# Optimization experiments

Hardware: AMD Instinct MI355X
Metric: run time of the kernel (lower is better)

## Reference

```python
import jax, jax.numpy as jnp
import numpy as np

B, S, H, NH = 2, 2048, 2048, 16
HD = H // NH
SCALE = 1.0 / np.sqrt(HD).astype(np.float32)


def setup_inputs() -> dict:
    key = jax.random.key(0)
    ks = jax.random.split(key, 11)
    std = 1.0 / np.sqrt(H)
    inp = {
        'query': jax.random.normal(ks[0], (B, S, H), dtype=jnp.float32),
        'key': jax.random.normal(ks[1], (B, S, H), dtype=jnp.float32),
        'value': jax.random.normal(ks[2], (B, S, H), dtype=jnp.float32),
        'Wq': jax.random.normal(ks[3], (H, H), dtype=jnp.float32) * std,
        'bq': jax.random.normal(ks[4], (H,), dtype=jnp.float32) * std,
        'Wk': jax.random.normal(ks[5], (H, H), dtype=jnp.float32) * std,
        'bk': jax.random.normal(ks[6], (H,), dtype=jnp.float32) * std,
        'Wv': jax.random.normal(ks[7], (H, H), dtype=jnp.float32) * std,
        'bv': jax.random.normal(ks[8], (H,), dtype=jnp.float32) * std,
        'Wo': jax.random.normal(ks[9], (H, H), dtype=jnp.float32) * std,
        'bo': jax.random.normal(ks[10], (H,), dtype=jnp.float32) * std,
    }
    return inp


def reference(query, key, value, Wq, bq, Wk, bk, Wv, bv, Wo, bo):
    # Linear projections (torch Linear: x @ W.T + b)
    q = query @ Wq.T + bq
    k = key @ Wk.T + bk
    v = value @ Wv.T + bv
    # [B, NH, S, HD]
    q = q.reshape(B, S, NH, HD).transpose(0, 2, 1, 3)
    k = k.reshape(B, S, NH, HD).transpose(0, 2, 1, 3)
    v = v.reshape(B, S, NH, HD).transpose(0, 2, 1, 3)
    scores = jnp.einsum('bhqd,bhkd->bhqk', q, k) * SCALE
    attn = jax.nn.softmax(scores, axis=-1)  # dropout p=0 (eval)
    ctx = jnp.einsum('bhqk,bhkd->bhqd', attn, v)
    ctx = ctx.transpose(0, 2, 1, 3).reshape(B, S, H)
    out = ctx @ Wo.T + bo
    return out
```

## Files before the change

kernel.cpp:

```cpp
#include <hip/hip_runtime.h>


typedef __bf16 bf16_t;
typedef __bf16 bf16x8 __attribute__((ext_vector_type(8)));
typedef float  f32x4  __attribute__((ext_vector_type(4)));

#define DEVI __device__ __forceinline__

DEVI void async_copy16(const void* gsrc, void* ldst) {
  __builtin_amdgcn_global_load_lds(
      (const __attribute__((address_space(1))) unsigned int*)gsrc,
      (__attribute__((address_space(3))) unsigned int*)ldst, 16, 0, 0);
}

constexpr int Bc = 2, Sc = 2048, Hc = 2048, NHc = 16, HDc = 128;
constexpr float SCALE_F = 0.088388347648318447f;
constexpr int PSTR = 72;

DEVI void cast_body(const float* __restrict__ in, bf16_t* __restrict__ out) {
  int i = (blockIdx.x * 256 + threadIdx.x) * 8;
  float4 f0 = *(const float4*)(in + i);
  float4 f1 = *(const float4*)(in + i + 4);
  union { bf16_t h[8]; uint4 u; } o;
  o.h[0] = (bf16_t)f0.x; o.h[1] = (bf16_t)f0.y;
  o.h[2] = (bf16_t)f0.z; o.h[3] = (bf16_t)f0.w;
  o.h[4] = (bf16_t)f1.x; o.h[5] = (bf16_t)f1.y;
  o.h[6] = (bf16_t)f1.z; o.h[7] = (bf16_t)f1.w;
  *(uint4*)(out + i) = o.u;
}

__global__ void cast3(const float* __restrict__ a, const float* __restrict__ b,
                      const float* __restrict__ c, bf16_t* __restrict__ oa,
                      bf16_t* __restrict__ ob, bf16_t* __restrict__ oc) {
  const float* src = blockIdx.y == 0 ? a : blockIdx.y == 1 ? b : c;
  bf16_t* dst = blockIdx.y == 0 ? oa : blockIdx.y == 1 ? ob : oc;
  cast_body(src, dst);
}

__global__ void cast4(const float* __restrict__ a, const float* __restrict__ b,
                      const float* __restrict__ c, const float* __restrict__ d,
                      bf16_t* __restrict__ oa, bf16_t* __restrict__ ob,
                      bf16_t* __restrict__ oc, bf16_t* __restrict__ od) {
  const float* src = blockIdx.y == 0 ? a : blockIdx.y == 1 ? b
                   : blockIdx.y == 2 ? c : d;
  bf16_t* dst = blockIdx.y == 0 ? oa : blockIdx.y == 1 ? ob
              : blockIdx.y == 2 ? oc : od;
  cast_body(src, dst);
}

template <int M, int N, int K, int OUT_MODE>
__global__ __launch_bounds__(512, 2) void gemm_bt(const bf16_t* __restrict__ A,
                                                  const bf16_t* __restrict__ Bw,
                                                  const float* __restrict__ bias,
                                                  void* __restrict__ Cout,
                                                  float scale) {
  constexpr int BM = 256, BN = 128, BK = 64;
  constexpr int NT = K / BK;
  constexpr int SLOT = (BM + BN) * BK;
  __shared__ __align__(16) bf16_t lds[3 * SLOT];

  const int tid = threadIdx.x;
  const int lane = tid & 63;
  const int wave = tid >> 6;
  const int bm = blockIdx.x & (M / BM - 1);
  const int bn = blockIdx.x / (M / BM);
  const int wm = wave >> 1, wn = wave & 1;
  const int quad = lane >> 4, l15 = lane & 15;

  const bf16_t* Abase = A + (size_t)bm * BM * K;
  const bf16_t* Bbase = Bw + (size_t)bn * BN * K;
  const bf16_t* asrc0; const bf16_t* asrc1; const bf16_t* asrc2; const bf16_t* asrc3;
  const bf16_t* bsrc0; const bf16_t* bsrc1;
  int aoff0, aoff1, aoff2, aoff3, boff0, boff1;
  {
    int i0 = wave * 4;
    int r0 = i0 * 8 + (lane >> 3);       aoff0 = i0 * 512;
    int r1 = (i0 + 1) * 8 + (lane >> 3); aoff1 = (i0 + 1) * 512;
    int r2 = (i0 + 2) * 8 + (lane >> 3); aoff2 = (i0 + 2) * 512;
    int r3 = (i0 + 3) * 8 + (lane >> 3); aoff3 = (i0 + 3) * 512;
    asrc0 = Abase + (size_t)r0 * K + (((lane & 7) ^ (r0 & 7)) * 8);
    asrc1 = Abase + (size_t)r1 * K + (((lane & 7) ^ (r1 & 7)) * 8);
    asrc2 = Abase + (size_t)r2 * K + (((lane & 7) ^ (r2 & 7)) * 8);
    asrc3 = Abase + (size_t)r3 * K + (((lane & 7) ^ (r3 & 7)) * 8);
    int j0 = wave * 2;
    int s0 = j0 * 8 + (lane >> 3);       boff0 = BM * BK + j0 * 512;
    int s1 = (j0 + 1) * 8 + (lane >> 3); boff1 = BM * BK + (j0 + 1) * 512;
    bsrc0 = Bbase + (size_t)s0 * K + (((lane & 7) ^ (s0 & 7)) * 8);
    bsrc1 = Bbase + (size_t)s1 * K + (((lane & 7) ^ (s1 & 7)) * 8);
  }

  f32x4 zero4 = {0.f, 0.f, 0.f, 0.f};
  f32x4 acc[4][4];
#pragma unroll
  for (int i = 0; i < 4; ++i)
#pragma unroll
    for (int j = 0; j < 4; ++j) acc[i][j] = zero4;

  int arow[4], brow[4];
#pragma unroll
  for (int t = 0; t < 4; ++t) {
    arow[t] = wm * 64 + t * 16 + l15;
    brow[t] = wn * 64 + t * 16 + l15;
  }

  auto stage_half0 = [&](int kt) {
    bf16_t* slot = lds + (kt % 3) * SLOT;
    int k0 = kt * BK;
    async_copy16(asrc0 + k0, slot + aoff0);
    async_copy16(asrc1 + k0, slot + aoff1);
    async_copy16(bsrc0 + k0, slot + boff0);
  };
  auto stage_half1 = [&](int kt) {
    bf16_t* slot = lds + (kt % 3) * SLOT;
    int k0 = kt * BK;
    async_copy16(asrc2 + k0, slot + aoff2);
    async_copy16(asrc3 + k0, slot + aoff3);
    async_copy16(bsrc1 + k0, slot + boff1);
  };

  stage_half0(0); stage_half1(0);
  stage_half0(1); stage_half1(1);

  for (int kt = 0; kt < NT; ++kt) {
    if (kt + 1 < NT) {
      asm volatile("s_waitcnt vmcnt(6)" ::: "memory");
    } else {
      asm volatile("s_waitcnt vmcnt(0)" ::: "memory");
    }
    __builtin_amdgcn_s_barrier();
    asm volatile("" ::: "memory");

    const bf16_t* As = lds + (kt % 3) * SLOT;
    const bf16_t* Bs = As + BM * BK;
    const bool do_stage = (kt + 2 < NT);

#pragma unroll
    for (int ks = 0; ks < 2; ++ks) {
      if (do_stage) {
        if (ks == 0) stage_half0(kt + 2);
        else         stage_half1(kt + 2);
      }
      bf16x8 af[4], bfv[4];
#pragma unroll
      for (int mt = 0; mt < 4; ++mt)
        af[mt] = *(const bf16x8*)(As + arow[mt] * 64 +
                                  (((ks * 4 + quad) ^ (arow[mt] & 7)) * 8));
#pragma unroll
      for (int nt = 0; nt < 4; ++nt)
        bfv[nt] = *(const bf16x8*)(Bs + brow[nt] * 64 +
                                   (((ks * 4 + quad) ^ (brow[nt] & 7)) * 8));
      __builtin_amdgcn_s_setprio(1);
#pragma unroll
      for (int mt = 0; mt < 4; ++mt)
#pragma unroll
        for (int nt = 0; nt < 4; ++nt)
          acc[mt][nt] = __builtin_amdgcn_mfma_f32_16x16x32_bf16(
              af[mt], bfv[nt], acc[mt][nt], 0, 0, 0);
      __builtin_amdgcn_s_setprio(0);
    }
  }

  float bv[4];
#pragma unroll
  for (int nt = 0; nt < 4; ++nt) bv[nt] = bias[bn * BN + brow[nt]];

#pragma unroll
  for (int mt = 0; mt < 4; ++mt) {
    const int rbase = bm * BM + wm * 64 + mt * 16 + quad * 4;
#pragma unroll
    for (int nt = 0; nt < 4; ++nt) {
      const int col = bn * BN + brow[nt];
      if constexpr (OUT_MODE == 0) {
        bf16_t* C = (bf16_t*)Cout;
#pragma unroll
        for (int r = 0; r < 4; ++r)
          C[(size_t)(rbase + r) * N + col] = (bf16_t)((acc[mt][nt][r] + bv[nt]) * scale);
      } else if constexpr (OUT_MODE == 2) {
        float* C = (float*)Cout;
#pragma unroll
        for (int r = 0; r < 4; ++r)
          C[(size_t)(rbase + r) * N + col] = acc[mt][nt][r] + bv[nt];
      } else {
        bf16_t* C = (bf16_t*)Cout;
        const int bb = rbase >> 11;
        const int s0 = rbase & (Sc - 1);
        const int h = col >> 7, d = col & (HDc - 1);
        union { bf16_t h4[4]; uint2 u; } o;
#pragma unroll
        for (int r = 0; r < 4; ++r) o.h4[r] = (bf16_t)(acc[mt][nt][r] + bv[nt]);
        *(uint2*)(C + (((size_t)(bb * NHc + h) * HDc + d) * Sc + s0)) = o.u;
      }
    }
  }
}

__global__ __launch_bounds__(256, 2) void flash_attn(const bf16_t* __restrict__ Q,
                                                     const bf16_t* __restrict__ Kg,
                                                     const bf16_t* __restrict__ Vt,
                                                     bf16_t* __restrict__ ctx) {
  __shared__ __align__(16) bf16_t smem[64 * 128 + 128 * 64 + 4 * 32 * PSTR];
  bf16_t* Ks = smem;
  bf16_t* Vs = smem + 8192;
  bf16_t* Ps = smem + 16384;

  const int tid = threadIdx.x, lane = tid & 63, wave = tid >> 6;
  const int quad = lane >> 4, l15 = lane & 15;
  const int bid = blockIdx.x;
  const int qt = bid & 15, h = (bid >> 4) & 15, b = bid >> 8;

  bf16_t* Pw = Ps + wave * (32 * PSTR);

  bf16x8 qf[2][4];
#pragma unroll
  for (int mt = 0; mt < 2; ++mt) {
    int grow = b * Sc + qt * 128 + wave * 32 + mt * 16 + l15;
    const bf16_t* qp = Q + (size_t)grow * Hc + h * HDc;
#pragma unroll
    for (int kc = 0; kc < 4; ++kc) qf[mt][kc] = *(const bf16x8*)(qp + kc * 32 + quad * 8);
  }

  f32x4 zero4 = {0.f, 0.f, 0.f, 0.f};
  f32x4 o[2][8];
#pragma unroll
  for (int mt = 0; mt < 2; ++mt)
#pragma unroll
    for (int dt = 0; dt < 8; ++dt) o[mt][dt] = zero4;
  float mrow[2][4], lrow[2][4];
#pragma unroll
  for (int mt = 0; mt < 2; ++mt)
#pragma unroll
    for (int r = 0; r < 4; ++r) { mrow[mt][r] = -1e30f; lrow[mt][r] = 0.f; }

  int kr_[4], kc_[4], vr_[4], vc_[4];
#pragma unroll
  for (int i = 0; i < 4; ++i) {
    int s = wave * 4 + i;
    kr_[i] = s * 4 + quad;        kc_[i] = l15 ^ (kr_[i] & 7);
    vr_[i] = s * 8 + (lane >> 3); vc_[i] = (lane & 7) ^ (vr_[i] & 7);
  }
  const bf16_t* Kbase = Kg + (size_t)b * Sc * Hc + h * HDc;
  const bf16_t* Vbase = Vt + (size_t)(b * NHc + h) * HDc * Sc;

  for (int kb = 0; kb < 32; ++kb) {
#pragma unroll
    for (int i = 0; i < 4; ++i) {
      int s = wave * 4 + i;
      async_copy16(Kbase + (size_t)(kb * 64 + kr_[i]) * Hc + kc_[i] * 8, Ks + s * 512);
      async_copy16(Vbase + (size_t)vr_[i] * Sc + kb * 64 + vc_[i] * 8, Vs + s * 512);
    }
    __syncthreads();

    f32x4 sf[2][4];
#pragma unroll
    for (int mt = 0; mt < 2; ++mt)
#pragma unroll
      for (int nt = 0; nt < 4; ++nt) sf[mt][nt] = zero4;
#pragma unroll
    for (int kc = 0; kc < 4; ++kc)
#pragma unroll
      for (int nt = 0; nt < 4; ++nt) {
        int kr = nt * 16 + l15;
        bf16x8 kf = *(const bf16x8*)(Ks + kr * 128 + (((kc * 4 + quad) ^ (kr & 7)) * 8));
        sf[0][nt] = __builtin_amdgcn_mfma_f32_16x16x32_bf16(qf[0][kc], kf, sf[0][nt], 0, 0, 0);
        sf[1][nt] = __builtin_amdgcn_mfma_f32_16x16x32_bf16(qf[1][kc], kf, sf[1][nt], 0, 0, 0);
      }

#pragma unroll
    for (int mt = 0; mt < 2; ++mt)
#pragma unroll
      for (int r = 0; r < 4; ++r) {
        float mx = sf[mt][0][r];
#pragma unroll
        for (int nt = 1; nt < 4; ++nt) mx = fmaxf(mx, sf[mt][nt][r]);
#pragma unroll
        for (int off = 1; off < 16; off <<= 1) mx = fmaxf(mx, __shfl_xor(mx, off));
        float mnew = fmaxf(mrow[mt][r], mx);
        float alpha = __expf(mrow[mt][r] - mnew);
        float rs = 0.f;
#pragma unroll
        for (int nt = 0; nt < 4; ++nt) {
          float p = __expf(sf[mt][nt][r] - mnew);
          sf[mt][nt][r] = p;
          rs += p;
        }
#pragma unroll
        for (int off = 1; off < 16; off <<= 1) rs += __shfl_xor(rs, off);
        lrow[mt][r] = lrow[mt][r] * alpha + rs;
        mrow[mt][r] = mnew;
#pragma unroll
        for (int dt = 0; dt < 8; ++dt) o[mt][dt][r] *= alpha;
      }

#pragma unroll
    for (int mt = 0; mt < 2; ++mt)
#pragma unroll
      for (int nt = 0; nt < 4; ++nt)
#pragma unroll
        for (int r = 0; r < 4; ++r)
          Pw[(mt * 16 + quad * 4 + r) * PSTR + nt * 16 + l15] = (bf16_t)sf[mt][nt][r];

    bf16x8 pf[2][2];
#pragma unroll
    for (int mt = 0; mt < 2; ++mt) {
      const bf16_t* pr = Pw + (mt * 16 + l15) * PSTR;
#pragma unroll
      for (int kc = 0; kc < 2; ++kc)
        pf[mt][kc] = *(const bf16x8*)(pr + kc * 32 + quad * 8);
    }

#pragma unroll
    for (int kc = 0; kc < 2; ++kc)
#pragma unroll
      for (int dt = 0; dt < 8; ++dt) {
        int vr = dt * 16 + l15;
        bf16x8 vf = *(const bf16x8*)(Vs + vr * 64 + (((kc * 4 + quad) ^ (vr & 7)) * 8));
        o[0][dt] = __builtin_amdgcn_mfma_f32_16x16x32_bf16(pf[0][kc], vf, o[0][dt], 0, 0, 0);
        o[1][dt] = __builtin_amdgcn_mfma_f32_16x16x32_bf16(pf[1][kc], vf, o[1][dt], 0, 0, 0);
      }
    __syncthreads();
  }

  __syncthreads();
  bf16_t* Ow = smem + wave * 4096;
#pragma unroll
  for (int mt = 0; mt < 2; ++mt) {
    float rinv[4];
#pragma unroll
    for (int r = 0; r < 4; ++r) rinv[r] = 1.f / lrow[mt][r];
#pragma unroll
    for (int dt = 0; dt < 8; ++dt)
#pragma unroll
      for (int r = 0; r < 4; ++r)
        Ow[(mt * 16 + quad * 4 + r) * 128 + dt * 16 + l15] = (bf16_t)(o[mt][dt][r] * rinv[r]);
  }
#pragma unroll
  for (int r = 0; r < 32; ++r) {
    unsigned v = *(const unsigned*)(Ow + r * 128 + lane * 2);
    int grow = b * Sc + qt * 128 + wave * 32 + r;
    *(unsigned*)(ctx + (size_t)grow * Hc + h * HDc + lane * 2) = v;
  }
}

extern "C" void kernel_launch(void* const* d_in, const int* in_sizes, int n_in,
                              void* d_out, int out_size, void* d_ws, size_t ws_size,
                              hipStream_t stream) {
  const float* query = (const float*)d_in[0];
  const float* key_i = (const float*)d_in[1];
  const float* value = (const float*)d_in[2];
  const float* Wq = (const float*)d_in[3];
  const float* bq = (const float*)d_in[4];
  const float* Wk = (const float*)d_in[5];
  const float* bk = (const float*)d_in[6];
  const float* Wv = (const float*)d_in[7];
  const float* bv = (const float*)d_in[8];
  const float* Wo = (const float*)d_in[9];
  const float* bo = (const float*)d_in[10];

  const size_t XE = (size_t)Bc * Sc * Hc;
  const size_t WE = (size_t)Hc * Hc;
  const size_t need = 6 * XE * 2 + 4 * WE * 2;
  if (ws_size < need) return;

  char* ws = (char*)d_ws;
  size_t off = 0;
  auto alloc = [&](size_t bytes) {
    char* p = ws + off;
    off += (bytes + 255) & ~(size_t)255;
    return p;
  };
  bf16_t* Xq = (bf16_t*)alloc(XE * 2);
  bf16_t* Xk = (bf16_t*)alloc(XE * 2);
  bf16_t* Xv = (bf16_t*)alloc(XE * 2);
  bf16_t* Wqb = (bf16_t*)alloc(WE * 2);
  bf16_t* Wkb = (bf16_t*)alloc(WE * 2);
  bf16_t* Wvb = (bf16_t*)alloc(WE * 2);
  bf16_t* Wob = (bf16_t*)alloc(WE * 2);
  bf16_t* qb = (bf16_t*)alloc(XE * 2);
  bf16_t* kb = (bf16_t*)alloc(XE * 2);
  bf16_t* vtb = (bf16_t*)alloc(XE * 2);
  bf16_t* ctxb = Xq;

  cast3<<<dim3((unsigned)(XE / 2048), 3), 256, 0, stream>>>(query, key_i, value, Xq, Xk, Xv);
  cast4<<<dim3((unsigned)(WE / 2048), 4), 256, 0, stream>>>(Wq, Wk, Wv, Wo, Wqb, Wkb, Wvb, Wob);

  gemm_bt<4096, 2048, 2048, 0><<<256, 512, 0, stream>>>(Xq, Wqb, bq, qb, SCALE_F);
  gemm_bt<4096, 2048, 2048, 0><<<256, 512, 0, stream>>>(Xk, Wkb, bk, kb, 1.0f);
  gemm_bt<4096, 2048, 2048, 1><<<256, 512, 0, stream>>>(Xv, Wvb, bv, vtb, 1.0f);

  flash_attn<<<512, 256, 0, stream>>>(qb, kb, vtb, ctxb);

  gemm_bt<4096, 2048, 2048, 2><<<256, 512, 0, stream>>>(ctxb, Wob, bo, (float*)d_out, 1.0f);
}
```

Before: 474.4 us.

## Merge QKV GEMMs into one launch and pipeline flash attention with lazy rescaling

The three Q/K/V projection GEMMs become a single launch with a 3-way grid, which fills the GPU with 768 blocks instead of three 256-block waves. Flash attention double-buffers K tiles and prefetches the next V tile behind the PV matmul, using explicit vmcnt waits and barriers. The softmax now runs in base 2 with log2e folded into the Q scale, skips the rescale unless the row max grows by more than 8, and defers the cross-lane row-sum reduction to the end. It costs more LDS and turns the GEMM output mode into a runtime branch, and the hand-counted vmcnt values are fragile.

```diff
diff --git a/kernel.cpp b/kernel.cpp
--- a/kernel.cpp
+++ b/kernel.cpp
@@ -14,7 +14,7 @@
 }
 
 constexpr int Bc = 2, Sc = 2048, Hc = 2048, NHc = 16, HDc = 128;
-constexpr float SCALE_F = 0.088388347648318447f;
+constexpr float SCALE_LOG2E = 0.12751744550358464f;
 constexpr int PSTR = 72;
 
 DEVI void cast_body(const float* __restrict__ in, bf16_t* __restrict__ out) {
@@ -48,12 +48,10 @@
   cast_body(src, dst);
 }
 
-template <int M, int N, int K, int OUT_MODE>
-__global__ __launch_bounds__(512, 2) void gemm_bt(const bf16_t* __restrict__ A,
-                                                  const bf16_t* __restrict__ Bw,
-                                                  const float* __restrict__ bias,
-                                                  void* __restrict__ Cout,
-                                                  float scale) {
+template <int M, int N, int K>
+DEVI void gemm_body(const bf16_t* __restrict__ A, const bf16_t* __restrict__ Bw,
+                    const float* __restrict__ bias, void* __restrict__ Cout,
+                    float scale, int out_mode) {
   constexpr int BM = 256, BN = 128, BK = 64;
   constexpr int NT = K / BK;
   constexpr int SLOT = (BM + BN) * BK;
@@ -170,12 +168,12 @@
 #pragma unroll
     for (int nt = 0; nt < 4; ++nt) {
       const int col = bn * BN + brow[nt];
-      if constexpr (OUT_MODE == 0) {
+      if (out_mode == 0) {
         bf16_t* C = (bf16_t*)Cout;
 #pragma unroll
         for (int r = 0; r < 4; ++r)
           C[(size_t)(rbase + r) * N + col] = (bf16_t)((acc[mt][nt][r] + bv[nt]) * scale);
-      } else if constexpr (OUT_MODE == 2) {
+      } else if (out_mode == 2) {
         float* C = (float*)Cout;
 #pragma unroll
         for (int r = 0; r < 4; ++r)
@@ -194,14 +192,37 @@
   }
 }
 
+__global__ __launch_bounds__(512, 2) void qkv_proj(
+    const bf16_t* __restrict__ Xq, const bf16_t* __restrict__ Xk,
+    const bf16_t* __restrict__ Xv, const bf16_t* __restrict__ Wq,
+    const bf16_t* __restrict__ Wk, const bf16_t* __restrict__ Wv,
+    const float* __restrict__ bq, const float* __restrict__ bk,
+    const float* __restrict__ bv, bf16_t* __restrict__ q,
+    bf16_t* __restrict__ k, bf16_t* __restrict__ vt) {
+  const int p = blockIdx.y;
+  const bf16_t* A = p == 0 ? Xq : p == 1 ? Xk : Xv;
+  const bf16_t* W = p == 0 ? Wq : p == 1 ? Wk : Wv;
+  const float* bi = p == 0 ? bq : p == 1 ? bk : bv;
+  void* out = p == 0 ? (void*)q : p == 1 ? (void*)k : (void*)vt;
+  gemm_body<4096, 2048, 2048>(A, W, bi, out, p == 0 ? SCALE_LOG2E : 1.0f,
+                              p == 2 ? 1 : 0);
+}
+
+__global__ __launch_bounds__(512, 2) void o_proj(
+    const bf16_t* __restrict__ A, const bf16_t* __restrict__ W,
+    const float* __restrict__ bi, float* __restrict__ out) {
+  gemm_body<4096, 2048, 2048>(A, W, bi, out, 1.0f, 2);
+}
+
 __global__ __launch_bounds__(256, 2) void flash_attn(const bf16_t* __restrict__ Q,
                                                      const bf16_t* __restrict__ Kg,
                                                      const bf16_t* __restrict__ Vt,
                                                      bf16_t* __restrict__ ctx) {
-  __shared__ __align__(16) bf16_t smem[64 * 128 + 128 * 64 + 4 * 32 * PSTR];
-  bf16_t* Ks = smem;
-  bf16_t* Vs = smem + 8192;
-  bf16_t* Ps = smem + 16384;
+  __shared__ __align__(16) bf16_t smem[2 * 64 * 128 + 128 * 64 + 4 * 32 * PSTR];
+  bf16_t* Ks0 = smem;
+  bf16_t* Ks1 = smem + 8192;
+  bf16_t* Vs = smem + 16384;
+  bf16_t* Ps = smem + 24576;
 
   const int tid = threadIdx.x, lane = tid & 63, wave = tid >> 6;
   const int quad = lane >> 4, l15 = lane & 15;
@@ -225,11 +246,11 @@
   for (int mt = 0; mt < 2; ++mt)
 #pragma unroll
     for (int dt = 0; dt < 8; ++dt) o[mt][dt] = zero4;
-  float mrow[2][4], lrow[2][4];
+  float mrow[2][4], lpart[2][4];
 #pragma unroll
   for (int mt = 0; mt < 2; ++mt)
 #pragma unroll
-    for (int r = 0; r < 4; ++r) { mrow[mt][r] = -1e30f; lrow[mt][r] = 0.f; }
+    for (int r = 0; r < 4; ++r) { mrow[mt][r] = -1e30f; lpart[mt][r] = 0.f; }
 
   int kr_[4], kc_[4], vr_[4], vc_[4];
 #pragma unroll
@@ -241,14 +262,30 @@
   const bf16_t* Kbase = Kg + (size_t)b * Sc * Hc + h * HDc;
   const bf16_t* Vbase = Vt + (size_t)(b * NHc + h) * HDc * Sc;
 
+  auto stageK = [&](int kb, bf16_t* dst) {
+#pragma unroll
+    for (int i = 0; i < 4; ++i)
+      async_copy16(Kbase + (size_t)(kb * 64 + kr_[i]) * Hc + kc_[i] * 8,
+                   dst + (wave * 4 + i) * 512);
+  };
+  auto stageV = [&](int kb) {
+#pragma unroll
+    for (int i = 0; i < 4; ++i)
+      async_copy16(Vbase + (size_t)vr_[i] * Sc + kb * 64 + vc_[i] * 8,
+                   Vs + (wave * 4 + i) * 512);
+  };
+
+  stageK(0, Ks0);
+  stageV(0);
+  stageK(1, Ks1);
+
   for (int kb = 0; kb < 32; ++kb) {
-#pragma unroll
-    for (int i = 0; i < 4; ++i) {
-      int s = wave * 4 + i;
-      async_copy16(Kbase + (size_t)(kb * 64 + kr_[i]) * Hc + kc_[i] * 8, Ks + s * 512);
-      async_copy16(Vbase + (size_t)vr_[i] * Sc + kb * 64 + vc_[i] * 8, Vs + s * 512);
-    }
-    __syncthreads();
+    bf16_t* Kcur = (kb & 1) ? Ks1 : Ks0;
+
+    if (kb + 1 < 32) asm volatile("s_waitcnt vmcnt(8)" ::: "memory");
+    else             asm volatile("s_waitcnt vmcnt(4)" ::: "memory");
+    __builtin_amdgcn_s_barrier();
+    asm volatile("" ::: "memory");
 
     f32x4 sf[2][4];
 #pragma unroll
@@ -260,35 +297,48 @@
 #pragma unroll
       for (int nt = 0; nt < 4; ++nt) {
         int kr = nt * 16 + l15;
-        bf16x8 kf = *(const bf16x8*)(Ks + kr * 128 + (((kc * 4 + quad) ^ (kr & 7)) * 8));
+        bf16x8 kf = *(const bf16x8*)(Kcur + kr * 128 + (((kc * 4 + quad) ^ (kr & 7)) * 8));
         sf[0][nt] = __builtin_amdgcn_mfma_f32_16x16x32_bf16(qf[0][kc], kf, sf[0][nt], 0, 0, 0);
         sf[1][nt] = __builtin_amdgcn_mfma_f32_16x16x32_bf16(qf[1][kc], kf, sf[1][nt], 0, 0, 0);
       }
 
+    float mx[2][4];
+    bool need = false;
 #pragma unroll
     for (int mt = 0; mt < 2; ++mt)
 #pragma unroll
       for (int r = 0; r < 4; ++r) {
-        float mx = sf[mt][0][r];
-#pragma unroll
-        for (int nt = 1; nt < 4; ++nt) mx = fmaxf(mx, sf[mt][nt][r]);
-#pragma unroll
-        for (int off = 1; off < 16; off <<= 1) mx = fmaxf(mx, __shfl_xor(mx, off));
-        float mnew = fmaxf(mrow[mt][r], mx);
-        float alpha = __expf(mrow[mt][r] - mnew);
-        float rs = 0.f;
-#pragma unroll
-        for (int nt = 0; nt < 4; ++nt) {
-          float p = __expf(sf[mt][nt][r] - mnew);
-          sf[mt][nt][r] = p;
-          rs += p;
+        float m0 = fmaxf(fmaxf(sf[mt][0][r], sf[mt][1][r]),
+                         fmaxf(sf[mt][2][r], sf[mt][3][r]));
+#pragma unroll
+        for (int off = 1; off < 16; off <<= 1) m0 = fmaxf(m0, __shfl_xor(m0, off));
+        mx[mt][r] = m0;
+        need = need || (m0 > mrow[mt][r] + 8.0f);
+      }
+    if (__any(need)) {
+#pragma unroll
+      for (int mt = 0; mt < 2; ++mt)
+#pragma unroll
+        for (int r = 0; r < 4; ++r) {
+          float mnew = fmaxf(mrow[mt][r], mx[mt][r]);
+          float alpha = __builtin_amdgcn_exp2f(mrow[mt][r] - mnew);
+          mrow[mt][r] = mnew;
+          lpart[mt][r] *= alpha;
+#pragma unroll
+          for (int dt = 0; dt < 8; ++dt) o[mt][dt][r] *= alpha;
         }
-#pragma unroll
-        for (int off = 1; off < 16; off <<= 1) rs += __shfl_xor(rs, off);
-        lrow[mt][r] = lrow[mt][r] * alpha + rs;
-        mrow[mt][r] = mnew;
-#pragma unroll
-        for (int dt = 0; dt < 8; ++dt) o[mt][dt][r] *= alpha;
+    }
+#pragma unroll
+    for (int mt = 0; mt < 2; ++mt)
+#pragma unroll
+      for (int r = 0; r < 4; ++r) {
+        float p0 = __builtin_amdgcn_exp2f(sf[mt][0][r] - mrow[mt][r]);
+        float p1 = __builtin_amdgcn_exp2f(sf[mt][1][r] - mrow[mt][r]);
+        float p2 = __builtin_amdgcn_exp2f(sf[mt][2][r] - mrow[mt][r]);
+        float p3 = __builtin_amdgcn_exp2f(sf[mt][3][r] - mrow[mt][r]);
+        sf[mt][0][r] = p0; sf[mt][1][r] = p1;
+        sf[mt][2][r] = p2; sf[mt][3][r] = p3;
+        lpart[mt][r] += (p0 + p1) + (p2 + p3);
       }
 
 #pragma unroll
@@ -307,6 +357,11 @@
       for (int kc = 0; kc < 2; ++kc)
         pf[mt][kc] = *(const bf16x8*)(pr + kc * 32 + quad * 8);
     }
+
+    if (kb + 1 < 32) asm volatile("s_waitcnt vmcnt(4)" ::: "memory");
+    else             asm volatile("s_waitcnt vmcnt(0)" ::: "memory");
+    __builtin_amdgcn_s_barrier();
+    asm volatile("" ::: "memory");
 
 #pragma unroll
     for (int kc = 0; kc < 2; ++kc)
@@ -317,7 +372,11 @@
         o[0][dt] = __builtin_amdgcn_mfma_f32_16x16x32_bf16(pf[0][kc], vf, o[0][dt], 0, 0, 0);
         o[1][dt] = __builtin_amdgcn_mfma_f32_16x16x32_bf16(pf[1][kc], vf, o[1][dt], 0, 0, 0);
       }
-    __syncthreads();
+
+    __builtin_amdgcn_s_barrier();
+    asm volatile("" ::: "memory");
+    if (kb + 1 < 32) stageV(kb + 1);
+    if (kb + 2 < 32) stageK(kb + 2, Kcur);
   }
 
   __syncthreads();
@@ -326,7 +385,12 @@
   for (int mt = 0; mt < 2; ++mt) {
     float rinv[4];
 #pragma unroll
-    for (int r = 0; r < 4; ++r) rinv[r] = 1.f / lrow[mt][r];
+    for (int r = 0; r < 4; ++r) {
+      float l = lpart[mt][r];
+#pragma unroll
+      for (int off = 1; off < 16; off <<= 1) l += __shfl_xor(l, off);
+      rinv[r] = 1.f / l;
+    }
 #pragma unroll
     for (int dt = 0; dt < 8; ++dt)
 #pragma unroll
@@ -383,11 +447,10 @@
   cast3<<<dim3((unsigned)(XE / 2048), 3), 256, 0, stream>>>(query, key_i, value, Xq, Xk, Xv);
   cast4<<<dim3((unsigned)(WE / 2048), 4), 256, 0, stream>>>(Wq, Wk, Wv, Wo, Wqb, Wkb, Wvb, Wob);
 
-  gemm_bt<4096, 2048, 2048, 0><<<256, 512, 0, stream>>>(Xq, Wqb, bq, qb, SCALE_F);
-  gemm_bt<4096, 2048, 2048, 0><<<256, 512, 0, stream>>>(Xk, Wkb, bk, kb, 1.0f);
-  gemm_bt<4096, 2048, 2048, 1><<<256, 512, 0, stream>>>(Xv, Wvb, bv, vtb, 1.0f);
+  qkv_proj<<<dim3(256, 3), 512, 0, stream>>>(Xq, Xk, Xv, Wqb, Wkb, Wvb,
+                                             bq, bk, bv, qb, kb, vtb);
 
   flash_attn<<<512, 256, 0, stream>>>(qb, kb, vtb, ctxb);
 
-  gemm_bt<4096, 2048, 2048, 2><<<256, 512, 0, stream>>>(ctxb, Wob, bo, (float*)d_out, 1.0f);
-}
+  o_proj<<<256, 512, 0, stream>>>(ctxb, Wob, bo, (float*)d_out);
+}
```

New measurement: 462.8 us. 2.4% less time.
